# Optimization experiments

Hardware: AMD Instinct MI355X
Metric: run time of the kernel (lower is better)

The kernel has to match this reference:

```python
import jax, jax.numpy as jnp
import numpy as np
import math

DIM = 1024

def setup_inputs() -> dict:
    key = jax.random.key(0)
    ks = jax.random.split(key, 5)
    X = jax.random.normal(ks[0], (4, 2048, DIM), dtype=jnp.float32)
    # Linear params (stored as [in, out] so y = x @ W + b)
    W_in = jax.random.normal(ks[1], (DIM, 3 * DIM), dtype=jnp.float32) / math.sqrt(DIM)
    b_in = jnp.zeros((3 * DIM,), dtype=jnp.float32)
    W_out = jax.random.normal(ks[2], (DIM, DIM), dtype=jnp.float32) / math.sqrt(DIM)
    b_out = jnp.zeros((DIM,), dtype=jnp.float32)
    return {"X": X, "W_in": W_in, "b_in": b_in, "W_out": W_out, "b_out": b_out}

def reference(X, W_in, b_in, W_out, b_out):
    dim = X.shape[-1]
    QKV = X @ W_in + b_in                       # [B, S, 3*dim]
    Q, K, V = jnp.split(QKV, 3, axis=-1)        # each [B, S, dim]
    scores = jnp.einsum('bqd,bkd->bqk', Q, K) / math.sqrt(dim)  # [B, S, S]
    attn = jax.nn.softmax(scores, axis=-1)
    out = jnp.einsum('bqk,bkd->bqd', attn, V)   # [B, S, dim]
    return out @ W_out + b_out
```

## Files before the change

### kernel.cpp

```cpp
#include <hip/hip_runtime.h>
#include <hip/hip_bf16.h>
#include <math.h>

typedef __attribute__((ext_vector_type(8))) __bf16 bf16x8;
typedef __attribute__((ext_vector_type(4))) float f32x4;

#define DIM 1024
#define SEQ 2048
#define BATCH 4
#define ROWS (BATCH*SEQ)

#define BAR() do { asm volatile("" ::: "memory"); __builtin_amdgcn_s_barrier(); asm volatile("" ::: "memory"); } while(0)
#define WAITV(n) asm volatile("s_waitcnt vmcnt(" #n ")" ::: "memory")
#define SCHED0() __builtin_amdgcn_sched_barrier(0)

__device__ __forceinline__ unsigned short f2bf(float f) {
  unsigned int u = __float_as_uint(f);
  u += 0x7FFF + ((u >> 16) & 1);
  return (unsigned short)(u >> 16);
}
__device__ __forceinline__ unsigned short to_bf_bits(float v) { return f2bf(v); }
__device__ __forceinline__ unsigned short to_bf_bits(unsigned short v) { return v; }

__device__ __forceinline__ void gload_lds16(const void* g, void* lds) {
  __builtin_amdgcn_global_load_lds((__attribute__((address_space(1))) void*)g,
                                   (__attribute__((address_space(3))) void*)lds,
                                   16, 0, 0);
}

__global__ __launch_bounds__(256)
void conv_f32_bf16(const float* __restrict__ src, unsigned short* __restrict__ dst, int n8) {
  int i = blockIdx.x * blockDim.x + threadIdx.x;
  if (i >= n8) return;
  const float4* s = reinterpret_cast<const float4*>(src) + (size_t)i * 2;
  float4 a = s[0], b = s[1];
  union { unsigned short h[8]; uint4 v; } p;
  p.h[0]=f2bf(a.x); p.h[1]=f2bf(a.y); p.h[2]=f2bf(a.z); p.h[3]=f2bf(a.w);
  p.h[4]=f2bf(b.x); p.h[5]=f2bf(b.y); p.h[6]=f2bf(b.z); p.h[7]=f2bf(b.w);
  reinterpret_cast<uint4*>(dst)[i] = p.v;
}

template<typename Tin>
__global__ __launch_bounds__(1024)
void transpose_conv(const Tin* __restrict__ src, int ldsrc, size_t sstride,
                    unsigned short* __restrict__ dst, int lddst, size_t dstride) {
  __shared__ unsigned short tile[32][33];
  const Tin* s = src + (size_t)blockIdx.z * sstride;
  unsigned short* d = dst + (size_t)blockIdx.z * dstride;
  int tx = threadIdx.x, ty = threadIdx.y;
  int r = blockIdx.y * 32 + ty, c = blockIdx.x * 32 + tx;
  tile[ty][tx] = to_bf_bits(s[(size_t)r * ldsrc + c]);
  __syncthreads();
  d[(size_t)(blockIdx.x * 32 + ty) * lddst + blockIdx.y * 32 + tx] = tile[tx][ty];
}

template<int NREP, int NLO, int MB, int NBASE>
__device__ __forceinline__ void quad(f32x4 (&acc)[8][NREP], const bf16x8 (&af)[4][2],
                                     const bf16x8 (&bg)[NLO][2]) {
#pragma unroll
  for (int kk = 0; kk < 2; ++kk)
#pragma unroll
    for (int m = 0; m < 4; ++m)
#pragma unroll
      for (int n = 0; n < NLO; ++n)
        acc[MB + m][NBASE + n] =
            __builtin_amdgcn_mfma_f32_16x16x32_bf16(af[m][kk], bg[n][kk], acc[MB + m][NBASE + n], 0, 0, 0);
}

#define EPI_QKV 0
#define EPI_F32 1
#define EPI_BF16 2
#define EPI_BIAS_F32 3

template<int BN, int EPI>
__global__ __launch_bounds__(512, 2)
void gemm8(const unsigned short* __restrict__ A, int lda, size_t sA,
           const unsigned short* __restrict__ B, int ldb, size_t sB,
           void* __restrict__ C, int ldc, size_t sC,
           const float* __restrict__ bias, int K) {
  constexpr int NREP = BN / 64;
  constexpr int NLO = NREP / 2;
  constexpr int NW = 16 * NREP;
  __shared__ unsigned short As[2 * 256 * 64];
  __shared__ unsigned short Bs[2 * BN * 64];

  const int tid = threadIdx.x;
  const int lane = tid & 63, wave = tid >> 6;
  const int wm = wave >> 2, wn = wave & 3;
  const int fr = lane & 15, fk = lane >> 4;
  const int tileM = blockIdx.y * 256, tileN = blockIdx.x * BN;
  const unsigned short* Ab = A + (size_t)blockIdx.z * sA;
  const unsigned short* Bb = B + (size_t)blockIdx.z * sB;

  const int srow = tid >> 3;
  const int sg = (tid & 7) ^ (srow & 7);

  auto stageA = [&](int buf, int half, int k0) {
#pragma unroll
    for (int q = 0; q < 2; ++q) {
      int rl = half * 128 + q * 64 + srow;
      gload_lds16(Ab + (size_t)(tileM + rl) * lda + k0 + sg * 8,
                  &As[buf * (256 * 64) + (half * 128 + q * 64) * 64 + tid * 8]);
    }
  };
  auto stageB = [&](int buf, int part, int k0) {
#pragma unroll
    for (int q = 0; q < 2; ++q) {
      int rl = part * 128 + q * 64 + srow;
      gload_lds16(Bb + (size_t)(tileN + rl) * ldb + k0 + sg * 8,
                  &Bs[buf * (BN * 64) + (part * 128 + q * 64) * 64 + tid * 8]);
    }
  };

  f32x4 acc[8][NREP];
#pragma unroll
  for (int m = 0; m < 8; ++m)
#pragma unroll
    for (int n = 0; n < NREP; ++n) acc[m][n] = (f32x4){0.f, 0.f, 0.f, 0.f};

  const int NS = K >> 6;
  stageA(0, 0, 0); stageA(0, 1, 0); stageB(0, 0, 0);
  if (BN == 256) stageB(0, 1, 0);
  stageA(1, 0, 64);

  bf16x8 afLo[4][2], afHi[4][2], bgLo[NLO][2], bgHi[NLO][2];

  for (int t = 0; t < NS; ++t) {
    const int cb = t & 1, nb = cb ^ 1;
    const unsigned short* Asl = &As[cb * (256 * 64)];
    const unsigned short* Bsl = &Bs[cb * (BN * 64)];
    const int k1 = (t + 1) << 6, k2 = (t + 2) << 6;

    if (t + 1 < NS) { WAITV(2); } else { WAITV(0); }
    BAR();
#pragma unroll
    for (int m = 0; m < 4; ++m) {
      int rl = wm * 128 + m * 16 + fr;
#pragma unroll
      for (int kk = 0; kk < 2; ++kk)
        afLo[m][kk] = *(const bf16x8*)&Asl[rl * 64 + (((kk * 4 + fk) ^ (rl & 7)) << 3)];
    }
#pragma unroll
    for (int n = 0; n < NLO; ++n) {
      int rl = wn * NW + n * 16 + fr;
#pragma unroll
      for (int kk = 0; kk < 2; ++kk)
        bgLo[n][kk] = *(const bf16x8*)&Bsl[rl * 64 + (((kk * 4 + fk) ^ (rl & 7)) << 3)];
    }
    if (t + 1 < NS) stageA(nb, 1, k1);
    BAR(); SCHED0();
    __builtin_amdgcn_s_setprio(1);
    quad<NREP, NLO, 0, 0>(acc, afLo, bgLo);
    __builtin_amdgcn_s_setprio(0); SCHED0();
    BAR();

#pragma unroll
    for (int n = 0; n < NLO; ++n) {
      int rl = wn * NW + (NLO + n) * 16 + fr;
#pragma unroll
      for (int kk = 0; kk < 2; ++kk)
        bgHi[n][kk] = *(const bf16x8*)&Bsl[rl * 64 + (((kk * 4 + fk) ^ (rl & 7)) << 3)];
    }
    if (t + 1 < NS) stageB(nb, 0, k1);
    BAR(); SCHED0();
    __builtin_amdgcn_s_setprio(1);
    quad<NREP, NLO, 0, NLO>(acc, afLo, bgHi);
    __builtin_amdgcn_s_setprio(0); SCHED0();
    BAR();

#pragma unroll
    for (int m = 0; m < 4; ++m) {
      int rl = wm * 128 + (4 + m) * 16 + fr;
#pragma unroll
      for (int kk = 0; kk < 2; ++kk)
        afHi[m][kk] = *(const bf16x8*)&Asl[rl * 64 + (((kk * 4 + fk) ^ (rl & 7)) << 3)];
    }
    if (BN == 256) { if (t + 1 < NS) stageB(nb, 1, k1); }
    BAR(); SCHED0();
    __builtin_amdgcn_s_setprio(1);
    quad<NREP, NLO, 4, 0>(acc, afHi, bgLo);
    __builtin_amdgcn_s_setprio(0); SCHED0();
    BAR();

    if (t + 2 < NS) stageA(cb, 0, k2);
    BAR(); SCHED0();
    __builtin_amdgcn_s_setprio(1);
    quad<NREP, NLO, 4, NLO>(acc, afHi, bgHi);
    __builtin_amdgcn_s_setprio(0); SCHED0();
    BAR();
  }

#pragma unroll
  for (int m = 0; m < 8; ++m)
#pragma unroll
    for (int n = 0; n < NREP; ++n)
#pragma unroll
      for (int j = 0; j < 4; ++j) {
        int row = tileM + wm * 128 + m * 16 + fk * 4 + j;
        int col = tileN + wn * NW + n * 16 + fr;
        float v = acc[m][n][j];
        if (EPI == EPI_QKV) {
          v += bias[col];
          if (col < DIM) v *= 0.03125f;
          ((unsigned short*)C + (size_t)blockIdx.z * sC)[(size_t)row * ldc + col] = f2bf(v);
        } else if (EPI == EPI_BF16) {
          ((unsigned short*)C + (size_t)blockIdx.z * sC)[(size_t)row * ldc + col] = f2bf(v);
        } else if (EPI == EPI_BIAS_F32) {
          ((float*)C + (size_t)blockIdx.z * sC)[(size_t)row * ldc + col] = v + bias[col];
        } else {
          ((float*)C + (size_t)blockIdx.z * sC)[(size_t)row * ldc + col] = v;
        }
      }
}

__global__ __launch_bounds__(256)
void softmax_kernel(float* __restrict__ S, size_t zstride) {
  __shared__ float red[8];
  float* row = S + (size_t)blockIdx.y * zstride + (size_t)blockIdx.x * SEQ;
  const int tid = threadIdx.x;
  const int lane = tid & 63, wave = tid >> 6;
  const float4* src = reinterpret_cast<const float4*>(row) + tid * 2;
  float4 a = src[0], b = src[1];
  float v[8] = {a.x, a.y, a.z, a.w, b.x, b.y, b.z, b.w};
  float m = v[0];
#pragma unroll
  for (int i = 1; i < 8; ++i) m = fmaxf(m, v[i]);
  for (int o = 32; o; o >>= 1) m = fmaxf(m, __shfl_xor(m, o));
  if (lane == 0) red[wave] = m;
  __syncthreads();
  m = fmaxf(fmaxf(red[0], red[1]), fmaxf(red[2], red[3]));
  float e[8], s = 0.f;
#pragma unroll
  for (int i = 0; i < 8; ++i) { e[i] = expf(v[i] - m); s += e[i]; }
  for (int o = 32; o; o >>= 1) s += __shfl_xor(s, o);
  if (lane == 0) red[4 + wave] = s;
  __syncthreads();
  s = red[4] + red[5] + red[6] + red[7];
  float inv = 1.f / s;
  union { unsigned short h[8]; uint4 u; } p;
#pragma unroll
  for (int i = 0; i < 8; ++i) p.h[i] = f2bf(e[i] * inv);
  reinterpret_cast<uint4*>(row)[tid] = p.u;
}

extern "C" void kernel_launch(void* const* d_in, const int* in_sizes, int n_in,
                              void* d_out, int out_size, void* d_ws, size_t ws_size,
                              hipStream_t stream) {
  const float* X     = (const float*)d_in[0];
  const float* W_in  = (const float*)d_in[1];
  const float* b_in  = (const float*)d_in[2];
  const float* W_out = (const float*)d_in[3];
  const float* b_out = (const float*)d_in[4];
  float* out = (float*)d_out;
  char* ws = (char*)d_ws;

  size_t o = 0;
  auto alloc = [&](size_t bytes) { size_t r = o; o += (bytes + 255) & ~(size_t)255; return r; };
  unsigned short* Xbf   = (unsigned short*)(ws + alloc((size_t)ROWS * DIM * 2));
  unsigned short* WinT  = (unsigned short*)(ws + alloc((size_t)3 * DIM * DIM * 2));
  unsigned short* WoutT = (unsigned short*)(ws + alloc((size_t)DIM * DIM * 2));
  unsigned short* QKV   = (unsigned short*)(ws + alloc((size_t)ROWS * 3 * DIM * 2));
  size_t fixed = o;
  size_t per_batch = (((size_t)SEQ * SEQ * 4 + 255) & ~(size_t)255) +
                     (((size_t)DIM * SEQ * 2 + 255) & ~(size_t)255);
  int G = (ws_size >= fixed + 4 * per_batch) ? BATCH : 1;
  float*          Sc = (float*)(ws + alloc((size_t)G * SEQ * SEQ * 4));
  unsigned short* Vt = (unsigned short*)(ws + alloc((size_t)G * DIM * SEQ * 2));
  unsigned short* O  = Xbf;

  conv_f32_bf16<<<(ROWS * DIM / 8 + 255) / 256, 256, 0, stream>>>(X, Xbf, ROWS * DIM / 8);
  transpose_conv<float><<<dim3(3 * DIM / 32, DIM / 32, 1), dim3(32, 32), 0, stream>>>(
      W_in, 3 * DIM, 0, WinT, DIM, 0);
  transpose_conv<float><<<dim3(DIM / 32, DIM / 32, 1), dim3(32, 32), 0, stream>>>(
      W_out, DIM, 0, WoutT, DIM, 0);
  gemm8<256, EPI_QKV><<<dim3(3 * DIM / 256, ROWS / 256, 1), 512, 0, stream>>>(
      Xbf, DIM, 0, WinT, DIM, 0, QKV, 3 * DIM, 0, b_in, DIM);

  for (int b0 = 0; b0 < BATCH; b0 += G) {
    const unsigned short* Qb = QKV + (size_t)b0 * SEQ * 3 * DIM;
    const unsigned short* Kb = Qb + DIM;
    const unsigned short* Vb = Qb + 2 * DIM;
    transpose_conv<unsigned short><<<dim3(DIM / 32, SEQ / 32, G), dim3(32, 32), 0, stream>>>(
        Vb, 3 * DIM, (size_t)SEQ * 3 * DIM, Vt, SEQ, (size_t)DIM * SEQ);
    gemm8<256, EPI_F32><<<dim3(SEQ / 256, SEQ / 256, G), 512, 0, stream>>>(
        Qb, 3 * DIM, (size_t)SEQ * 3 * DIM, Kb, 3 * DIM, (size_t)SEQ * 3 * DIM,
        Sc, SEQ, (size_t)SEQ * SEQ, nullptr, DIM);
    softmax_kernel<<<dim3(SEQ, G), 256, 0, stream>>>(Sc, (size_t)SEQ * SEQ);
    gemm8<128, EPI_BF16><<<dim3(DIM / 128, SEQ / 256, G), 512, 0, stream>>>(
        (const unsigned short*)Sc, 2 * SEQ, (size_t)2 * SEQ * SEQ,
        Vt, SEQ, (size_t)DIM * SEQ,
        O + (size_t)b0 * SEQ * DIM, DIM, (size_t)SEQ * DIM, nullptr, SEQ);
  }
  gemm8<128, EPI_BIAS_F32><<<dim3(DIM / 128, ROWS / 256, 1), 512, 0, stream>>>(
      O, DIM, 0, WoutT, DIM, 0, out, DIM, 0, b_out, DIM);
}
```

Measured before the change: 244.5 us.

## Rewrite GEMM main loop with inline-asm LDS reads and BN=128 QKV tiles

Replaces the compiler-generated LDS fragment loads with inline ds_read_b128 using precomputed swizzled base addresses and immediate offsets. The vmcnt wait moves to the end of each iteration, with an explicit lgkmcnt wait before each MFMA phase. The BN=128 path now runs two MFMA phases per k-step instead of four, and the QKV projection switches to 128-wide tiles for more blocks. This is meant to cut address arithmetic and barrier count and to improve occupancy and overlap, but it relies on hand-managed waitcnt correctness.

```diff
diff --git a/kernel.cpp b/kernel.cpp
--- a/kernel.cpp
+++ b/kernel.cpp
@@ -4,6 +4,7 @@
 
 typedef __attribute__((ext_vector_type(8))) __bf16 bf16x8;
 typedef __attribute__((ext_vector_type(4))) float f32x4;
+typedef __attribute__((ext_vector_type(4))) unsigned int u32x4;
 
 #define DIM 1024
 #define SEQ 2048
@@ -12,7 +13,13 @@
 
 #define BAR() do { asm volatile("" ::: "memory"); __builtin_amdgcn_s_barrier(); asm volatile("" ::: "memory"); } while(0)
 #define WAITV(n) asm volatile("s_waitcnt vmcnt(" #n ")" ::: "memory")
+#define WAITL0() asm volatile("s_waitcnt lgkmcnt(0)" ::: "memory")
 #define SCHED0() __builtin_amdgcn_sched_barrier(0)
+#define PRIO(x) __builtin_amdgcn_s_setprio(x)
+
+#define DSR(d, a, off) do { u32x4 _t; \
+  asm volatile("ds_read_b128 %0, %1 offset:" #off : "=v"(_t) : "v"(a)); \
+  (d) = __builtin_bit_cast(bf16x8, _t); } while(0)
 
 __device__ __forceinline__ unsigned short f2bf(float f) {
   unsigned int u = __float_as_uint(f);
@@ -54,19 +61,6 @@
   d[(size_t)(blockIdx.x * 32 + ty) * lddst + blockIdx.y * 32 + tx] = tile[tx][ty];
 }
 
-template<int NREP, int NLO, int MB, int NBASE>
-__device__ __forceinline__ void quad(f32x4 (&acc)[8][NREP], const bf16x8 (&af)[4][2],
-                                     const bf16x8 (&bg)[NLO][2]) {
-#pragma unroll
-  for (int kk = 0; kk < 2; ++kk)
-#pragma unroll
-    for (int m = 0; m < 4; ++m)
-#pragma unroll
-      for (int n = 0; n < NLO; ++n)
-        acc[MB + m][NBASE + n] =
-            __builtin_amdgcn_mfma_f32_16x16x32_bf16(af[m][kk], bg[n][kk], acc[MB + m][NBASE + n], 0, 0, 0);
-}
-
 #define EPI_QKV 0
 #define EPI_F32 1
 #define EPI_BF16 2
@@ -79,7 +73,6 @@
            void* __restrict__ C, int ldc, size_t sC,
            const float* __restrict__ bias, int K) {
   constexpr int NREP = BN / 64;
-  constexpr int NLO = NREP / 2;
   constexpr int NW = 16 * NREP;
   __shared__ unsigned short As[2 * 256 * 64];
   __shared__ unsigned short Bs[2 * BN * 64];
@@ -119,75 +112,117 @@
     for (int n = 0; n < NREP; ++n) acc[m][n] = (f32x4){0.f, 0.f, 0.f, 0.f};
 
   const int NS = K >> 6;
+  const unsigned asb = (unsigned)(size_t)(__attribute__((address_space(3))) unsigned short*)As;
+  const unsigned bsb = (unsigned)(size_t)(__attribute__((address_space(3))) unsigned short*)Bs;
+  const unsigned aoff = (unsigned)((wm * 128 + fr) * 128 + ((fk ^ (fr & 7)) << 4));
+  const unsigned boff = (unsigned)((wn * NW + fr) * 128 + ((fk ^ (fr & 7)) << 4));
+
   stageA(0, 0, 0); stageA(0, 1, 0); stageB(0, 0, 0);
   if (BN == 256) stageB(0, 1, 0);
-  stageA(1, 0, 64);
-
-  bf16x8 afLo[4][2], afHi[4][2], bgLo[NLO][2], bgHi[NLO][2];
+  if (NS > 1) { stageA(1, 0, 64); WAITV(2); } else { WAITV(0); }
+  BAR();
+
+  bf16x8 afLo[4][2], afHi[4][2], bg[NREP][2];
 
   for (int t = 0; t < NS; ++t) {
-    const int cb = t & 1, nb = cb ^ 1;
-    const unsigned short* Asl = &As[cb * (256 * 64)];
-    const unsigned short* Bsl = &Bs[cb * (BN * 64)];
+    const unsigned aA0 = asb + ((t & 1) ? 32768u : 0u) + aoff;
+    const unsigned aA1 = aA0 ^ 64u;
+    const unsigned bB0 = bsb + ((t & 1) ? (unsigned)(BN * 128) : 0u) + boff;
+    const unsigned bB1 = bB0 ^ 64u;
     const int k1 = (t + 1) << 6, k2 = (t + 2) << 6;
-
-    if (t + 1 < NS) { WAITV(2); } else { WAITV(0); }
-    BAR();
-#pragma unroll
-    for (int m = 0; m < 4; ++m) {
-      int rl = wm * 128 + m * 16 + fr;
-#pragma unroll
-      for (int kk = 0; kk < 2; ++kk)
-        afLo[m][kk] = *(const bf16x8*)&Asl[rl * 64 + (((kk * 4 + fk) ^ (rl & 7)) << 3)];
+    const int nb = (t & 1) ^ 1;
+
+    if constexpr (BN == 256) {
+      DSR(afLo[0][0], aA0, 0); DSR(afLo[1][0], aA0, 2048); DSR(afLo[2][0], aA0, 4096); DSR(afLo[3][0], aA0, 6144);
+      DSR(afLo[0][1], aA1, 0); DSR(afLo[1][1], aA1, 2048); DSR(afLo[2][1], aA1, 4096); DSR(afLo[3][1], aA1, 6144);
+      DSR(bg[0][0], bB0, 0); DSR(bg[1][0], bB0, 2048);
+      DSR(bg[0][1], bB1, 0); DSR(bg[1][1], bB1, 2048);
+      if (t + 1 < NS) stageA(nb, 1, k1);
+      BAR(); WAITL0(); SCHED0();
+      PRIO(1);
+#pragma unroll
+      for (int kk = 0; kk < 2; ++kk)
+#pragma unroll
+        for (int m = 0; m < 4; ++m)
+#pragma unroll
+          for (int n = 0; n < 2; ++n)
+            acc[m][n] = __builtin_amdgcn_mfma_f32_16x16x32_bf16(afLo[m][kk], bg[n][kk], acc[m][n], 0, 0, 0);
+      PRIO(0); SCHED0();
+      BAR();
+      DSR(bg[2][0], bB0, 4096); DSR(bg[3][0], bB0, 6144);
+      DSR(bg[2][1], bB1, 4096); DSR(bg[3][1], bB1, 6144);
+      if (t + 1 < NS) stageB(nb, 0, k1);
+      BAR(); WAITL0(); SCHED0();
+      PRIO(1);
+#pragma unroll
+      for (int kk = 0; kk < 2; ++kk)
+#pragma unroll
+        for (int m = 0; m < 4; ++m)
+#pragma unroll
+          for (int n = 0; n < 2; ++n)
+            acc[m][2 + n] = __builtin_amdgcn_mfma_f32_16x16x32_bf16(afLo[m][kk], bg[2 + n][kk], acc[m][2 + n], 0, 0, 0);
+      PRIO(0); SCHED0();
+      BAR();
+      DSR(afHi[0][0], aA0, 8192); DSR(afHi[1][0], aA0, 10240); DSR(afHi[2][0], aA0, 12288); DSR(afHi[3][0], aA0, 14336);
+      DSR(afHi[0][1], aA1, 8192); DSR(afHi[1][1], aA1, 10240); DSR(afHi[2][1], aA1, 12288); DSR(afHi[3][1], aA1, 14336);
+      if (t + 1 < NS) stageB(nb, 1, k1);
+      BAR(); WAITL0(); SCHED0();
+      PRIO(1);
+#pragma unroll
+      for (int kk = 0; kk < 2; ++kk)
+#pragma unroll
+        for (int m = 0; m < 4; ++m)
+#pragma unroll
+          for (int n = 0; n < 2; ++n)
+            acc[4 + m][n] = __builtin_amdgcn_mfma_f32_16x16x32_bf16(afHi[m][kk], bg[n][kk], acc[4 + m][n], 0, 0, 0);
+      PRIO(0); SCHED0();
+      BAR();
+      if (t + 2 < NS) stageA(t & 1, 0, k2);
+      BAR();
+      PRIO(1);
+#pragma unroll
+      for (int kk = 0; kk < 2; ++kk)
+#pragma unroll
+        for (int m = 0; m < 4; ++m)
+#pragma unroll
+          for (int n = 0; n < 2; ++n)
+            acc[4 + m][2 + n] = __builtin_amdgcn_mfma_f32_16x16x32_bf16(afHi[m][kk], bg[2 + n][kk], acc[4 + m][2 + n], 0, 0, 0);
+      PRIO(0); SCHED0();
+      if (t + 1 < NS) { if (t + 2 < NS) { WAITV(2); } else { WAITV(0); } }
+      BAR();
+    } else {
+      DSR(afLo[0][0], aA0, 0); DSR(afLo[1][0], aA0, 2048); DSR(afLo[2][0], aA0, 4096); DSR(afLo[3][0], aA0, 6144);
+      DSR(afLo[0][1], aA1, 0); DSR(afLo[1][1], aA1, 2048); DSR(afLo[2][1], aA1, 4096); DSR(afLo[3][1], aA1, 6144);
+      DSR(bg[0][0], bB0, 0); DSR(bg[1][0], bB0, 2048);
+      DSR(bg[0][1], bB1, 0); DSR(bg[1][1], bB1, 2048);
+      if (t + 1 < NS) { stageA(nb, 1, k1); stageB(nb, 0, k1); }
+      BAR(); WAITL0(); SCHED0();
+      PRIO(1);
+#pragma unroll
+      for (int kk = 0; kk < 2; ++kk)
+#pragma unroll
+        for (int m = 0; m < 4; ++m)
+#pragma unroll
+          for (int n = 0; n < 2; ++n)
+            acc[m][n] = __builtin_amdgcn_mfma_f32_16x16x32_bf16(afLo[m][kk], bg[n][kk], acc[m][n], 0, 0, 0);
+      PRIO(0); SCHED0();
+      BAR();
+      DSR(afHi[0][0], aA0, 8192); DSR(afHi[1][0], aA0, 10240); DSR(afHi[2][0], aA0, 12288); DSR(afHi[3][0], aA0, 14336);
+      DSR(afHi[0][1], aA1, 8192); DSR(afHi[1][1], aA1, 10240); DSR(afHi[2][1], aA1, 12288); DSR(afHi[3][1], aA1, 14336);
+      if (t + 2 < NS) stageA(t & 1, 0, k2);
+      BAR(); WAITL0(); SCHED0();
+      PRIO(1);
+#pragma unroll
+      for (int kk = 0; kk < 2; ++kk)
+#pragma unroll
+        for (int m = 0; m < 4; ++m)
+#pragma unroll
+          for (int n = 0; n < 2; ++n)
+            acc[4 + m][n] = __builtin_amdgcn_mfma_f32_16x16x32_bf16(afHi[m][kk], bg[n][kk], acc[4 + m][n], 0, 0, 0);
+      PRIO(0); SCHED0();
+      if (t + 1 < NS) { if (t + 2 < NS) { WAITV(2); } else { WAITV(0); } }
+      BAR();
     }
-#pragma unroll
-    for (int n = 0; n < NLO; ++n) {
-      int rl = wn * NW + n * 16 + fr;
-#pragma unroll
-      for (int kk = 0; kk < 2; ++kk)
-        bgLo[n][kk] = *(const bf16x8*)&Bsl[rl * 64 + (((kk * 4 + fk) ^ (rl & 7)) << 3)];
-    }
-    if (t + 1 < NS) stageA(nb, 1, k1);
-    BAR(); SCHED0();
-    __builtin_amdgcn_s_setprio(1);
-    quad<NREP, NLO, 0, 0>(acc, afLo, bgLo);
-    __builtin_amdgcn_s_setprio(0); SCHED0();
-    BAR();
-
-#pragma unroll
-    for (int n = 0; n < NLO; ++n) {
-      int rl = wn * NW + (NLO + n) * 16 + fr;
-#pragma unroll
-      for (int kk = 0; kk < 2; ++kk)
-        bgHi[n][kk] = *(const bf16x8*)&Bsl[rl * 64 + (((kk * 4 + fk) ^ (rl & 7)) << 3)];
-    }
-    if (t + 1 < NS) stageB(nb, 0, k1);
-    BAR(); SCHED0();
-    __builtin_amdgcn_s_setprio(1);
-    quad<NREP, NLO, 0, NLO>(acc, afLo, bgHi);
-    __builtin_amdgcn_s_setprio(0); SCHED0();
-    BAR();
-
-#pragma unroll
-    for (int m = 0; m < 4; ++m) {
-      int rl = wm * 128 + (4 + m) * 16 + fr;
-#pragma unroll
-      for (int kk = 0; kk < 2; ++kk)
-        afHi[m][kk] = *(const bf16x8*)&Asl[rl * 64 + (((kk * 4 + fk) ^ (rl & 7)) << 3)];
-    }
-    if (BN == 256) { if (t + 1 < NS) stageB(nb, 1, k1); }
-    BAR(); SCHED0();
-    __builtin_amdgcn_s_setprio(1);
-    quad<NREP, NLO, 4, 0>(acc, afHi, bgLo);
-    __builtin_amdgcn_s_setprio(0); SCHED0();
-    BAR();
-
-    if (t + 2 < NS) stageA(cb, 0, k2);
-    BAR(); SCHED0();
-    __builtin_amdgcn_s_setprio(1);
-    quad<NREP, NLO, 4, NLO>(acc, afHi, bgHi);
-    __builtin_amdgcn_s_setprio(0); SCHED0();
-    BAR();
   }
 
 #pragma unroll
@@ -273,7 +308,7 @@
       W_in, 3 * DIM, 0, WinT, DIM, 0);
   transpose_conv<float><<<dim3(DIM / 32, DIM / 32, 1), dim3(32, 32), 0, stream>>>(
       W_out, DIM, 0, WoutT, DIM, 0);
-  gemm8<256, EPI_QKV><<<dim3(3 * DIM / 256, ROWS / 256, 1), 512, 0, stream>>>(
+  gemm8<128, EPI_QKV><<<dim3(3 * DIM / 128, ROWS / 256, 1), 512, 0, stream>>>(
       Xbf, DIM, 0, WinT, DIM, 0, QKV, 3 * DIM, 0, b_in, DIM);
 
   for (int b0 = 0; b0 < BATCH; b0 += G) {
```

New measurement: 230.4 us. 5.8% less time.
